# Performance work log

Measured on AMD Instinct MI355X. Metric: run time of the kernel, lower is better.

The kernel has to match this reference:

```python
import jax, jax.numpy as jnp
import numpy as np
from jax import lax

B, T, V, H, L = 4096, 256, 256, 20, 15  # batch, seq_len, one_hot_size, hidden_dim, MAX_LABEL


def setup_inputs() -> dict:
    key = jax.random.key(0)
    k0, k1, k2, k3 = jax.random.split(key, 4)
    return {
        "x": jax.random.randint(k0, (B, T), 0, V, dtype=jnp.int32),
        "drop_rate": jnp.float32(0.0),
        "kernel": jax.random.normal(k1, (V, 3 * H), dtype=jnp.float32) * 0.05,
        "recurrent_kernel": jax.random.normal(k2, (H, 3 * H), dtype=jnp.float32) * 0.05,
        "bias": jnp.zeros((2, 3 * H), dtype=jnp.float32),  # [input_bias, recurrent_bias] (reset_after=True)
        "dense_w": jax.random.normal(k3, (H, L), dtype=jnp.float32) * 0.05,
        "dense_b": jnp.zeros((L,), dtype=jnp.float32),
    }


def reference(x, drop_rate, kernel, recurrent_kernel, bias, dense_w, dense_b):
    # one_hot(x, 256) @ kernel is exactly a row-gather of kernel: same math, no 1GB one-hot.
    bi, br = bias[0], bias[1]
    xW = kernel[x] + bi  # [B, T, 3H]

    def step(h, xw_t):
        # Keras GRUCell, reset_after=True, gate order (z, r, h)
        hU = h @ recurrent_kernel + br                      # [B, 3H]
        xz, xr, xh = jnp.split(xw_t, 3, axis=-1)
        hz, hr, hh = jnp.split(hU, 3, axis=-1)
        z = jax.nn.sigmoid(xz + hz)
        r = jax.nn.sigmoid(xr + hr)
        h_cand = jnp.tanh(xh + r * hh)
        h_new = z * h + (1.0 - z) * h_cand
        return h_new, None

    h0 = jnp.zeros((x.shape[0], recurrent_kernel.shape[0]), dtype=kernel.dtype)
    hT, _ = lax.scan(step, h0, jnp.swapaxes(xW, 0, 1))     # scan over time, final state [B, H]

    # tf.nn.dropout: keep with prob 1-rate, scale kept values by 1/(1-rate).
    keep = 1.0 - drop_rate
    mask = jax.random.uniform(jax.random.key(42), hT.shape) >= drop_rate
    h_drop = jnp.where(mask, hT / keep, 0.0)

    logits = h_drop @ dense_w + dense_b                     # [B, 15]
    return logits
```

## Files before the change

### kernel.cpp

```cpp
#include <hip/hip_runtime.h>


#define BB 4096
#define TT 256
#define VV 256
#define HH 20
#define G3 60
#define LL 15
#define NBATCH 12
#define NTHREADS 256
#define HSTRIDE 24

typedef int v4i __attribute__((ext_vector_type(4)));
typedef int v2i __attribute__((ext_vector_type(2)));

__device__ __forceinline__ unsigned short f2bf(float f) {
    union { float f; unsigned int i; } c;
    c.f = f;
    unsigned int x = c.i;
    return (unsigned short)((x + 0x7FFFu + ((x >> 16) & 1u)) >> 16);
}

__device__ __forceinline__ unsigned pack2bf(float a, float b) {
    return (unsigned)f2bf(a) | ((unsigned)f2bf(b) << 16);
}

__device__ __forceinline__ float fast_rcp(float x) {
#if __has_builtin(__builtin_amdgcn_rcpf)
    return __builtin_amdgcn_rcpf(x);
#else
    return 1.0f / x;
#endif
}

__device__ __forceinline__ float fast_sigmoid(float x) {
    return fast_rcp(1.0f + __expf(-x));
}

__device__ __forceinline__ float fast_tanh(float x) {
    return 1.0f - 2.0f * fast_rcp(1.0f + __expf(2.0f * x));
}

__device__ __forceinline__ float dot2bf(unsigned a, unsigned b, float c) {
    float d;
    asm("v_dot2_f32_bf16 %0, %1, %2, %3" : "=v"(d) : "v"(a), "v"(b), "v"(c));
    return d;
}

__device__ __forceinline__ void h_exchange(unsigned waddr, unsigned hbf,
                                           unsigned raddr,
                                           v4i& p0, v4i& p1, v2i& p2) {
    asm volatile(
        "ds_write_b16 %3, %4\n\t"
        "ds_read_b128 %0, %5\n\t"
        "ds_read_b128 %1, %5 offset:16\n\t"
        "ds_read_b64 %2, %5 offset:32\n\t"
        "s_waitcnt lgkmcnt(0)"
        : "=&v"(p0), "=&v"(p1), "=&v"(p2)
        : "v"(waddr), "v"(hbf), "v"(raddr));
}

__global__ __launch_bounds__(NTHREADS, 1) void gru_kernel(
    const int* __restrict__ x,
    const float* __restrict__ kernelW,
    const float* __restrict__ rkernel,
    const float* __restrict__ bias,
    const float* __restrict__ dense_w,
    const float* __restrict__ dense_b,
    float* __restrict__ out)
{
    __shared__ int2  xwall[VV * HH];
    __shared__ float u_lds[HH * G3];
    __shared__ float w_lds[HH * LL];
    __shared__ float db_lds[LL];
    __shared__ int   x_lds[NBATCH][TT + 1];
    __shared__ unsigned short hbuf[NBATCH * HSTRIDE + 40];

    const int tid = threadIdx.x;
    const long b0 = (long)blockIdx.x * NBATCH;

    for (int idx = tid; idx < VV * HH; idx += NTHREADS) {
        const int v = idx / HH, j = idx - v * HH;
        const float vz = kernelW[v * G3 + j]          + bias[j];
        const float vr = kernelW[v * G3 + HH + j]     + bias[HH + j];
        const float vh = kernelW[v * G3 + 2 * HH + j] + bias[2 * HH + j];
        int2 pk;
        pk.x = (int)pack2bf(vz, vr);
        pk.y = __float_as_int(vh);
        xwall[idx] = pk;
    }
    for (int idx = tid; idx < HH * G3; idx += NTHREADS) u_lds[idx] = rkernel[idx];
    for (int idx = tid; idx < HH * LL; idx += NTHREADS) w_lds[idx] = dense_w[idx];
    if (tid < LL) db_lds[tid] = dense_b[tid];
    for (int k = tid; k < NBATCH * TT; k += NTHREADS) {
        const long gi = b0 * TT + k;
        x_lds[k >> 8][k & 255] = (gi < (long)BB * TT) ? x[gi] : 0;
    }
    for (int idx = tid; idx < NBATCH * HSTRIDE + 40; idx += NTHREADS)
        hbuf[idx] = 0;
    __syncthreads();

    const int lane = tid & 63;
    const int g3   = lane / 20;
    const int j    = lane - g3 * 20;
    const bool active = (lane < 60);
    const int lb   = (tid >> 6) * 3 + g3;
    const int lbc  = active ? lb : 0;

    const unsigned hbase = (unsigned)(size_t)&hbuf[0];
    const unsigned waddr = active
        ? hbase + 2u * (unsigned)(lb * HSTRIDE + j)
        : hbase + 2u * (unsigned)(NBATCH * HSTRIDE + (tid >> 6) * 8 + (lane - 60));
    const unsigned raddr = hbase + 2u * (unsigned)(HSTRIDE * lbc);

    unsigned Uz[10], Ur[10], Uh[10];
    #pragma unroll
    for (int q = 0; q < 10; ++q) {
        Uz[q] = pack2bf(u_lds[(2*q) * G3 + j],        u_lds[(2*q+1) * G3 + j]);
        Ur[q] = pack2bf(u_lds[(2*q) * G3 + HH + j],   u_lds[(2*q+1) * G3 + HH + j]);
        Uh[q] = pack2bf(u_lds[(2*q) * G3 + 2*HH + j], u_lds[(2*q+1) * G3 + 2*HH + j]);
    }
    #pragma unroll
    for (int q = 0; q < 10; ++q)
        asm volatile("" : "+v"(Uz[q]), "+v"(Ur[q]), "+v"(Uh[q]));

    const float brz = bias[G3 + j];
    const float brr = bias[G3 + HH + j];
    const float brh = bias[G3 + 2 * HH + j];

    float hmine = 0.0f;
    unsigned hbf = 0;
    const int* xrow = x_lds[lbc];

    #pragma unroll 2
    for (int t = 0; t < TT; ++t) {
        v4i p0, p1; v2i p2;
        h_exchange(waddr, hbf, raddr, p0, p1, p2);
        const unsigned hp[10] = { (unsigned)p0.x, (unsigned)p0.y, (unsigned)p0.z,
                                  (unsigned)p0.w, (unsigned)p1.x, (unsigned)p1.y,
                                  (unsigned)p1.z, (unsigned)p1.w, (unsigned)p2.x,
                                  (unsigned)p2.y };

        const int xv = xrow[t];
        const int2 w = xwall[xv * HH + j];
        const float xz = __uint_as_float(((unsigned)w.x) << 16);
        const float xr = __uint_as_float(((unsigned)w.x) & 0xffff0000u);
        const float xh = __int_as_float(w.y);

        float za = brz, ra = brr, ha = brh;
        float zb = 0.f, rb = 0.f, hb = 0.f;
        #pragma unroll
        for (int q = 0; q < 5; ++q) {
            za = dot2bf(hp[q], Uz[q], za);
            ra = dot2bf(hp[q], Ur[q], ra);
            ha = dot2bf(hp[q], Uh[q], ha);
        }
        #pragma unroll
        for (int q = 5; q < 10; ++q) {
            zb = dot2bf(hp[q], Uz[q], zb);
            rb = dot2bf(hp[q], Ur[q], rb);
            hb = dot2bf(hp[q], Uh[q], hb);
        }
        const float z  = fast_sigmoid(xz + (za + zb));
        const float r  = fast_sigmoid(xr + (ra + rb));
        const float hc = fast_tanh(fmaf(r, ha + hb, xh));
        hmine = hc + z * (hmine - hc);
        asm("v_cvt_pk_bf16_f32 %0, %1, %2" : "=v"(hbf) : "v"(hmine), "v"(hmine));
    }

    v4i p0, p1; v2i p2;
    h_exchange(waddr, hbf, raddr, p0, p1, p2);
    const unsigned fp[10] = { (unsigned)p0.x, (unsigned)p0.y, (unsigned)p0.z,
                              (unsigned)p0.w, (unsigned)p1.x, (unsigned)p1.y,
                              (unsigned)p1.z, (unsigned)p1.w, (unsigned)p2.x,
                              (unsigned)p2.y };
    float hf[HH];
    #pragma unroll
    for (int q = 0; q < 10; ++q) {
        hf[2*q]   = __uint_as_float(fp[q] << 16);
        hf[2*q+1] = __uint_as_float(fp[q] & 0xffff0000u);
    }

    const long gb = b0 + lb;
    if (active && j < LL && gb < BB) {
        float acc = db_lds[j];
        #pragma unroll
        for (int i = 0; i < HH; ++i)
            acc = fmaf(hf[i], w_lds[i * LL + j], acc);
        out[gb * LL + j] = acc;
    }
}

extern "C" void kernel_launch(void* const* d_in, const int* in_sizes, int n_in,
                              void* d_out, int out_size, void* d_ws, size_t ws_size,
                              hipStream_t stream) {
    const int* x            = (const int*)d_in[0];
    const float* kernelW    = (const float*)d_in[2];
    const float* rkernel    = (const float*)d_in[3];
    const float* bias       = (const float*)d_in[4];
    const float* dense_w    = (const float*)d_in[5];
    const float* dense_b    = (const float*)d_in[6];
    float* out              = (float*)d_out;

    dim3 grid((BB + NBATCH - 1) / NBATCH);
    dim3 block(NTHREADS);
    gru_kernel<<<grid, block, 0, stream>>>(x, kernelW, rkernel, bias,
                                           dense_w, dense_b, out);
}
```

Baseline: 85.78 us.

## Use single-wave blocks with direct global gathers and log2e-prescaled weights

Blocks shrink from 4 waves to 1 wave, each handling 3 batch rows. The large per-block LDS staging of the gathered input-weight table and the token ids is dropped; input projections are now read straight from global memory (cache-resident) and software-prefetched one step ahead. Recurrent weights and biases are prescaled by -log2(e) or 2·log2(e) so the activations can use raw v_exp_f32 with no extra multiply. This removes the heavy LDS prologue and raises occupancy, but puts global-load latency inside the serial time loop.

```diff
diff --git a/kernel.cpp b/kernel.cpp
--- a/kernel.cpp
+++ b/kernel.cpp
@@ -7,49 +7,42 @@
 #define HH 20
 #define G3 60
 #define LL 15
-#define NBATCH 12
-#define NTHREADS 256
-#define HSTRIDE 24
+#define L2E 1.44269504088896340736f
 
 typedef int v4i __attribute__((ext_vector_type(4)));
 typedef int v2i __attribute__((ext_vector_type(2)));
 
-__device__ __forceinline__ unsigned short f2bf(float f) {
-    union { float f; unsigned int i; } c;
-    c.f = f;
+static __device__ __forceinline__ unsigned short f2bf(float f) {
+    union { float f; unsigned int i; } c; c.f = f;
     unsigned int x = c.i;
     return (unsigned short)((x + 0x7FFFu + ((x >> 16) & 1u)) >> 16);
 }
-
-__device__ __forceinline__ unsigned pack2bf(float a, float b) {
+static __device__ __forceinline__ unsigned pack2bf(float a, float b) {
     return (unsigned)f2bf(a) | ((unsigned)f2bf(b) << 16);
 }
-
-__device__ __forceinline__ float fast_rcp(float x) {
+static __device__ __forceinline__ float fast_rcp(float x) {
 #if __has_builtin(__builtin_amdgcn_rcpf)
     return __builtin_amdgcn_rcpf(x);
 #else
     return 1.0f / x;
 #endif
 }
-
-__device__ __forceinline__ float fast_sigmoid(float x) {
-    return fast_rcp(1.0f + __expf(-x));
-}
-
-__device__ __forceinline__ float fast_tanh(float x) {
-    return 1.0f - 2.0f * fast_rcp(1.0f + __expf(2.0f * x));
-}
-
-__device__ __forceinline__ float dot2bf(unsigned a, unsigned b, float c) {
+static __device__ __forceinline__ float dot2bf(unsigned a, unsigned b, float c) {
     float d;
     asm("v_dot2_f32_bf16 %0, %1, %2, %3" : "=v"(d) : "v"(a), "v"(b), "v"(c));
     return d;
 }
-
-__device__ __forceinline__ void h_exchange(unsigned waddr, unsigned hbf,
-                                           unsigned raddr,
-                                           v4i& p0, v4i& p1, v2i& p2) {
+static __device__ __forceinline__ unsigned cvtpk(float a, float b) {
+    unsigned r;
+    asm("v_cvt_pk_bf16_f32 %0, %1, %2" : "=v"(r) : "v"(a), "v"(b));
+    return r;
+}
+static __device__ __forceinline__ float exp2i(float x) {
+    float r; asm("v_exp_f32 %0, %1" : "=v"(r) : "v"(x)); return r;
+}
+static __device__ __forceinline__ void h_exchange(unsigned waddr, unsigned hbf,
+                                                  unsigned raddr,
+                                                  v4i& p0, v4i& p1, v2i& p2) {
     asm volatile(
         "ds_write_b16 %3, %4\n\t"
         "ds_read_b128 %0, %5\n\t"
@@ -60,7 +53,7 @@
         : "v"(waddr), "v"(hbf), "v"(raddr));
 }
 
-__global__ __launch_bounds__(NTHREADS, 1) void gru_kernel(
+__global__ __launch_bounds__(64, 2) void gru_kernel(
     const int* __restrict__ x,
     const float* __restrict__ kernelW,
     const float* __restrict__ rkernel,
@@ -69,71 +62,57 @@
     const float* __restrict__ dense_b,
     float* __restrict__ out)
 {
-    __shared__ int2  xwall[VV * HH];
-    __shared__ float u_lds[HH * G3];
-    __shared__ float w_lds[HH * LL];
-    __shared__ float db_lds[LL];
-    __shared__ int   x_lds[NBATCH][TT + 1];
-    __shared__ unsigned short hbuf[NBATCH * HSTRIDE + 40];
+    __shared__ __align__(16) unsigned short hbuf[80];
 
-    const int tid = threadIdx.x;
-    const long b0 = (long)blockIdx.x * NBATCH;
+    const int lane = threadIdx.x;
+    const int g3a  = lane / 20;
+    const int g3   = (lane < 60) ? g3a : 0;
+    const int j    = lane - g3a * 20;
+    const bool active = (lane < 60);
+    const long b  = (long)blockIdx.x * 3 + g3;
+    const long bc = (b < BB) ? b : (BB - 1);
 
-    for (int idx = tid; idx < VV * HH; idx += NTHREADS) {
-        const int v = idx / HH, j = idx - v * HH;
-        const float vz = kernelW[v * G3 + j]          + bias[j];
-        const float vr = kernelW[v * G3 + HH + j]     + bias[HH + j];
-        const float vh = kernelW[v * G3 + 2 * HH + j] + bias[2 * HH + j];
-        int2 pk;
-        pk.x = (int)pack2bf(vz, vr);
-        pk.y = __float_as_int(vh);
-        xwall[idx] = pk;
-    }
-    for (int idx = tid; idx < HH * G3; idx += NTHREADS) u_lds[idx] = rkernel[idx];
-    for (int idx = tid; idx < HH * LL; idx += NTHREADS) w_lds[idx] = dense_w[idx];
-    if (tid < LL) db_lds[tid] = dense_b[tid];
-    for (int k = tid; k < NBATCH * TT; k += NTHREADS) {
-        const long gi = b0 * TT + k;
-        x_lds[k >> 8][k & 255] = (gi < (long)BB * TT) ? x[gi] : 0;
-    }
-    for (int idx = tid; idx < NBATCH * HSTRIDE + 40; idx += NTHREADS)
-        hbuf[idx] = 0;
-    __syncthreads();
-
-    const int lane = tid & 63;
-    const int g3   = lane / 20;
-    const int j    = lane - g3 * 20;
-    const bool active = (lane < 60);
-    const int lb   = (tid >> 6) * 3 + g3;
-    const int lbc  = active ? lb : 0;
+    if (lane < 40) *(int*)&hbuf[lane * 2] = 0;
 
     const unsigned hbase = (unsigned)(size_t)&hbuf[0];
-    const unsigned waddr = active
-        ? hbase + 2u * (unsigned)(lb * HSTRIDE + j)
-        : hbase + 2u * (unsigned)(NBATCH * HSTRIDE + (tid >> 6) * 8 + (lane - 60));
-    const unsigned raddr = hbase + 2u * (unsigned)(HSTRIDE * lbc);
+    const unsigned waddr = active ? (hbase + 48u * (unsigned)g3a + 2u * (unsigned)j)
+                                  : (hbase + 144u + 2u * (unsigned)(lane - 60));
+    const unsigned raddr = hbase + 48u * (unsigned)g3;
 
     unsigned Uz[10], Ur[10], Uh[10];
     #pragma unroll
     for (int q = 0; q < 10; ++q) {
-        Uz[q] = pack2bf(u_lds[(2*q) * G3 + j],        u_lds[(2*q+1) * G3 + j]);
-        Ur[q] = pack2bf(u_lds[(2*q) * G3 + HH + j],   u_lds[(2*q+1) * G3 + HH + j]);
-        Uh[q] = pack2bf(u_lds[(2*q) * G3 + 2*HH + j], u_lds[(2*q+1) * G3 + 2*HH + j]);
+        Uz[q] = pack2bf(rkernel[(2*q)*G3 + j]        * (-L2E),
+                        rkernel[(2*q+1)*G3 + j]      * (-L2E));
+        Ur[q] = pack2bf(rkernel[(2*q)*G3 + HH + j]   * (-L2E),
+                        rkernel[(2*q+1)*G3 + HH + j] * (-L2E));
+        Uh[q] = pack2bf(rkernel[(2*q)*G3 + 2*HH + j]   * (2.0f*L2E),
+                        rkernel[(2*q+1)*G3 + 2*HH + j] * (2.0f*L2E));
     }
-    #pragma unroll
-    for (int q = 0; q < 10; ++q)
-        asm volatile("" : "+v"(Uz[q]), "+v"(Ur[q]), "+v"(Uh[q]));
+    const float bzc = (bias[j]        + bias[G3 + j])      * (-L2E);
+    const float brc = (bias[HH + j]   + bias[G3 + HH + j]) * (-L2E);
+    const float bhi =  bias[2*HH + j]                      * (2.0f*L2E);
+    const float brh =  bias[G3 + 2*HH + j]                 * (2.0f*L2E);
 
-    const float brz = bias[G3 + j];
-    const float brr = bias[G3 + HH + j];
-    const float brh = bias[G3 + 2 * HH + j];
+    const int* xrow = x + bc * TT;
+
+    const int xv0 = xrow[0];
+    const float* kw0 = kernelW + xv0 * G3;
+    float cz = fmaf(kw0[j],        -L2E,     bzc);
+    float cr = fmaf(kw0[HH + j],   -L2E,     brc);
+    float ch = fmaf(kw0[2*HH + j], 2.0f*L2E, bhi);
+    int xvA = xrow[1];
 
     float hmine = 0.0f;
     unsigned hbf = 0;
-    const int* xrow = x_lds[lbc];
 
-    #pragma unroll 2
     for (int t = 0; t < TT; ++t) {
+        const float* kwn = kernelW + xvA * G3;
+        const float lz = kwn[j];
+        const float lr = kwn[HH + j];
+        const float lh = kwn[2*HH + j];
+        const int xvB = xrow[(t + 2 < TT) ? (t + 2) : (TT - 1)];
+
         v4i p0, p1; v2i p2;
         h_exchange(waddr, hbf, raddr, p0, p1, p2);
         const unsigned hp[10] = { (unsigned)p0.x, (unsigned)p0.y, (unsigned)p0.z,
@@ -141,13 +120,7 @@
                                   (unsigned)p1.z, (unsigned)p1.w, (unsigned)p2.x,
                                   (unsigned)p2.y };
 
-        const int xv = xrow[t];
-        const int2 w = xwall[xv * HH + j];
-        const float xz = __uint_as_float(((unsigned)w.x) << 16);
-        const float xr = __uint_as_float(((unsigned)w.x) & 0xffff0000u);
-        const float xh = __int_as_float(w.y);
-
-        float za = brz, ra = brr, ha = brh;
+        float za = cz,  ra = cr,  ha = brh;
         float zb = 0.f, rb = 0.f, hb = 0.f;
         #pragma unroll
         for (int q = 0; q < 5; ++q) {
@@ -161,11 +134,18 @@
             rb = dot2bf(hp[q], Ur[q], rb);
             hb = dot2bf(hp[q], Uh[q], hb);
         }
-        const float z  = fast_sigmoid(xz + (za + zb));
-        const float r  = fast_sigmoid(xr + (ra + rb));
-        const float hc = fast_tanh(fmaf(r, ha + hb, xh));
+
+        const float z  = fast_rcp(1.0f + exp2i(za + zb));
+        const float r  = fast_rcp(1.0f + exp2i(ra + rb));
+        const float yh = fmaf(r, ha + hb, ch);
+        const float hc = fmaf(-2.0f, fast_rcp(1.0f + exp2i(yh)), 1.0f);
         hmine = hc + z * (hmine - hc);
-        asm("v_cvt_pk_bf16_f32 %0, %1, %2" : "=v"(hbf) : "v"(hmine), "v"(hmine));
+        hbf = cvtpk(hmine, hmine);
+
+        cz = fmaf(lz, -L2E,     bzc);
+        cr = fmaf(lr, -L2E,     brc);
+        ch = fmaf(lh, 2.0f*L2E, bhi);
+        xvA = xvB;
     }
 
     v4i p0, p1; v2i p2;
@@ -181,13 +161,12 @@
         hf[2*q+1] = __uint_as_float(fp[q] & 0xffff0000u);
     }
 
-    const long gb = b0 + lb;
-    if (active && j < LL && gb < BB) {
-        float acc = db_lds[j];
+    if (active && j < LL && b < BB) {
+        float acc = dense_b[j];
         #pragma unroll
         for (int i = 0; i < HH; ++i)
-            acc = fmaf(hf[i], w_lds[i * LL + j], acc);
-        out[gb * LL + j] = acc;
+            acc = fmaf(hf[i], dense_w[i * LL + j], acc);
+        out[b * LL + j] = acc;
     }
 }
 
@@ -202,8 +181,8 @@
     const float* dense_b    = (const float*)d_in[6];
     float* out              = (float*)d_out;
 
-    dim3 grid((BB + NBATCH - 1) / NBATCH);
-    dim3 block(NTHREADS);
+    dim3 grid((BB + 2) / 3);
+    dim3 block(64);
     gru_kernel<<<grid, block, 0, stream>>>(x, kernelW, rkernel, bias,
                                            dense_w, dense_b, out);
 }
```

Result: faster. 83.40 us (-2.8%).
